# Performance work log

Measured on AMD Instinct MI355X. Metric: run time of the kernel, lower is better.

Reference implementation:

```python
import jax, jax.numpy as jnp
import numpy as np

DIM = 1024
HEADS = 8
DIM_HEAD = 64
DIM_INNER = HEADS * DIM_HEAD  # 512


def setup_inputs() -> dict:
    key = jax.random.key(0)
    k1, k2, k3, k4 = jax.random.split(key, 4)
    x = jax.random.normal(k1, (1, 4096, DIM), dtype=jnp.float32)
    gamma = jnp.ones((DIM,), dtype=jnp.float32)
    w_qkv = jax.random.normal(k2, (DIM, 3 * DIM_INNER), dtype=jnp.float32) * (DIM ** -0.5)
    w_out = jax.random.normal(k3, (DIM_INNER, DIM), dtype=jnp.float32) * (DIM_INNER ** -0.5)
    return {"x": x, "gamma": gamma, "w_qkv": w_qkv, "w_out": w_out}


def _rmsnorm(x, gamma):
    # F.normalize(x, dim=-1) * sqrt(dim) * gamma
    norm = jnp.sqrt(jnp.sum(x * x, axis=-1, keepdims=True))
    x = x / jnp.maximum(norm, 1e-12)
    return x * (DIM ** 0.5) * gamma


def reference(x, gamma, w_qkv, w_out):
    b, n, _ = x.shape
    h, d = HEADS, DIM_HEAD
    normed = _rmsnorm(x, gamma)
    qkv = normed @ w_qkv  # [b, n, 3*h*d]
    qkv = qkv.reshape(b, n, 3, h, d)
    q = jnp.transpose(qkv[:, :, 0], (0, 2, 1, 3))  # b h n d
    k = jnp.transpose(qkv[:, :, 1], (0, 2, 1, 3))
    v = jnp.transpose(qkv[:, :, 2], (0, 2, 1, 3))
    # default_attention (faithful: scales q by d**0.5 as in source)
    q = q * (d ** 0.5)
    sim = jnp.einsum('bhid,bhjd->bhij', q, k)
    mask_value = -jnp.finfo(sim.dtype).max
    causal_mask = jnp.triu(jnp.ones((n, n), dtype=bool), 1)
    sim = jnp.where(causal_mask, mask_value, sim)
    attn = jax.nn.softmax(sim, axis=-1)
    out = jnp.einsum('bhij,bhjd->bhid', attn, v)  # b h n d
    out = jnp.transpose(out, (0, 2, 1, 3)).reshape(b, n, h * d)
    return out @ w_out  # [b, n, dim]
```

## Files before the change

kernel.cpp:

```cpp
#include <hip/hip_runtime.h>
#include <math.h>

#define SEQ 4096
#define DIM 1024
#define HEADS 8
#define DINNER 512
#define QKVW 1536
#define PAD 80
#define CHUNK 16

typedef unsigned short u16;
typedef __attribute__((ext_vector_type(8))) short s8v;
typedef __attribute__((ext_vector_type(4))) float f4v;
#define MFMA(a, b, c) __builtin_amdgcn_mfma_f32_16x16x32_bf16(a, b, c, 0, 0, 0)

__device__ __forceinline__ u16 f2bf(float f) {
    unsigned u = __float_as_uint(f);
    u += 0x7fff + ((u >> 16) & 1);
    return (u16)(u >> 16);
}
__device__ __forceinline__ float bf2f(u16 b) { return __uint_as_float(((unsigned)b) << 16); }

__device__ __forceinline__ void gload16(const u16* g, u16* l) {
    __builtin_amdgcn_global_load_lds(
        (const __attribute__((address_space(1))) unsigned int*)g,
        (__attribute__((address_space(3))) unsigned int*)l, 16, 0, 0);
}

__device__ __forceinline__ int base16(int qt) {
    int a = qt >> 4, b = qt & 15;
    return 8 * a * (a + 1) + b * (a + 1);
}
__device__ __forceinline__ float* po_sel(int T, float* pd, float* pw) {
    return (T < 1024) ? pd + (size_t)T * 4096 : pw + (size_t)(T - 1024) * 4096;
}

__global__ __launch_bounds__(256) void rmsnorm_split(const float* __restrict__ x,
                                                     const float* __restrict__ gamma,
                                                     u16* __restrict__ hi,
                                                     u16* __restrict__ lo) {
    __shared__ float red[4];
    const int row = blockIdx.x, t = threadIdx.x;
    const float4 xv = ((const float4*)(x + (size_t)row * DIM))[t];
    float ss = xv.x * xv.x + xv.y * xv.y + xv.z * xv.z + xv.w * xv.w;
#pragma unroll
    for (int off = 32; off >= 1; off >>= 1) ss += __shfl_xor(ss, off, 64);
    if ((t & 63) == 0) red[t >> 6] = ss;
    __syncthreads();
    float scale = 32.0f / fmaxf(sqrtf(red[0] + red[1] + red[2] + red[3]), 1e-12f);
    const float4 gv = ((const float4*)gamma)[t];
    float y[4] = {xv.x * scale * gv.x, xv.y * scale * gv.y,
                  xv.z * scale * gv.z, xv.w * scale * gv.w};
    unsigned hw0, hw1, lw0, lw1;
    {
        u16 h0 = f2bf(y[0]), h1 = f2bf(y[1]), h2 = f2bf(y[2]), h3 = f2bf(y[3]);
        hw0 = (unsigned)h0 | ((unsigned)h1 << 16);
        hw1 = (unsigned)h2 | ((unsigned)h3 << 16);
        lw0 = (unsigned)f2bf(y[0] - bf2f(h0)) | ((unsigned)f2bf(y[1] - bf2f(h1)) << 16);
        lw1 = (unsigned)f2bf(y[2] - bf2f(h2)) | ((unsigned)f2bf(y[3] - bf2f(h3)) << 16);
    }
    *(uint2*)&hi[(size_t)row * DIM + t * 4] = make_uint2(hw0, hw1);
    *(uint2*)&lo[(size_t)row * DIM + t * 4] = make_uint2(lw0, lw1);
}

__global__ __launch_bounds__(256) void transpose_split(const float* __restrict__ in,
                                                       u16* __restrict__ hi,
                                                       u16* __restrict__ lo,
                                                       int R, int C, int want_lo) {
    __shared__ float tile[64][65];
    const int c0 = blockIdx.x * 64, r0 = blockIdx.y * 64;
    const int t = threadIdx.x, col = t & 63, rb = t >> 6;
#pragma unroll
    for (int j = 0; j < 16; ++j)
        tile[rb + j * 4][col] = in[(size_t)(r0 + rb + j * 4) * C + c0 + col];
    __syncthreads();
#pragma unroll
    for (int j = 0; j < 16; ++j) {
        int cc = rb + j * 4;
        float v = tile[col][cc];
        size_t oi = (size_t)(c0 + cc) * R + r0 + col;
        u16 h = f2bf(v);
        hi[oi] = h;
        if (want_lo) lo[oi] = f2bf(v - bf2f(h));
    }
}

__global__ __launch_bounds__(256) void gemm_qkv_128(
    const u16* __restrict__ Ah, const u16* __restrict__ Al,
    const u16* __restrict__ Bh, const u16* __restrict__ Bl,
    u16* __restrict__ qh, u16* __restrict__ ql,
    u16* __restrict__ kh, u16* __restrict__ kl, u16* __restrict__ vtp) {
    __shared__ __align__(16) u16 AsH[128 * 64], AsL[128 * 64];
    __shared__ __align__(16) u16 BsH[64 * 64], BsL[64 * 64];
    const int t = threadIdx.x;
    const int bn = blockIdx.x * 64, bm = blockIdx.y * 128;
    const int w = t >> 6, lane = t & 63, m = lane & 15, q = lane >> 4;
    const int wr = w >> 1, wc = w & 1;
    f4v acc[4][2];
#pragma unroll
    for (int i = 0; i < 4; ++i)
#pragma unroll
        for (int j = 0; j < 2; ++j) acc[i][j] = (f4v){0.f, 0.f, 0.f, 0.f};

    for (int k0 = 0; k0 < DIM; k0 += 64) {
        __syncthreads();
#pragma unroll
        for (int i = 0; i < 4; ++i) {
            int idx0 = i * 256 + w * 64;
            int row = (idx0 + lane) >> 3;
            int col = ((lane & 7) * 8) ^ ((row & 7) * 8);
            gload16(&Ah[(size_t)(bm + row) * DIM + k0 + col], &AsH[idx0 * 8]);
            gload16(&Al[(size_t)(bm + row) * DIM + k0 + col], &AsL[idx0 * 8]);
            if (i < 2) {
                gload16(&Bh[(size_t)(bn + row) * DIM + k0 + col], &BsH[idx0 * 8]);
                gload16(&Bl[(size_t)(bn + row) * DIM + k0 + col], &BsL[idx0 * 8]);
            }
        }
        __syncthreads();
#pragma unroll
        for (int kk = 0; kk < 64; kk += 32) {
            s8v a_h[4], a_l[4], b_h[2], b_l[2];
#pragma unroll
            for (int f = 0; f < 4; ++f) {
                int ar = wr * 64 + f * 16 + m;
                int ab = ar * 128 + (((kk + q * 8) * 2) ^ ((ar & 7) << 4));
                a_h[f] = *(const s8v*)((const char*)AsH + ab);
                a_l[f] = *(const s8v*)((const char*)AsL + ab);
            }
#pragma unroll
            for (int f = 0; f < 2; ++f) {
                int br = wc * 32 + f * 16 + m;
                int bb = br * 128 + (((kk + q * 8) * 2) ^ ((br & 7) << 4));
                b_h[f] = *(const s8v*)((const char*)BsH + bb);
                b_l[f] = *(const s8v*)((const char*)BsL + bb);
            }
#pragma unroll
            for (int fm = 0; fm < 4; ++fm)
#pragma unroll
                for (int fn = 0; fn < 2; ++fn) {
                    acc[fm][fn] = MFMA(a_h[fm], b_h[fn], acc[fm][fn]);
                    acc[fm][fn] = MFMA(a_l[fm], b_h[fn], acc[fm][fn]);
                    acc[fm][fn] = MFMA(a_h[fm], b_l[fn], acc[fm][fn]);
                }
        }
    }
    const int region = bn >> 9;
#pragma unroll
    for (int fm = 0; fm < 4; ++fm)
#pragma unroll
        for (int fn = 0; fn < 2; ++fn)
#pragma unroll
            for (int r = 0; r < 4; ++r) {
                int gr = bm + wr * 64 + fm * 16 + q * 4 + r;
                int gc = bn + wc * 32 + fn * 16 + m;
                float v = acc[fm][fn][r];
                if (region == 0) {
                    v *= 8.0f;
                    u16 h = f2bf(v);
                    qh[(size_t)gr * DINNER + gc] = h;
                    ql[(size_t)gr * DINNER + gc] = f2bf(v - bf2f(h));
                } else if (region == 1) {
                    u16 h = f2bf(v);
                    kh[(size_t)gr * DINNER + (gc - 512)] = h;
                    kl[(size_t)gr * DINNER + (gc - 512)] = f2bf(v - bf2f(h));
                } else {
                    vtp[(size_t)(gc - 1024) * SEQ + gr] = f2bf(v);
                }
            }
}

__global__ __launch_bounds__(256) void attn_chunk(
    const u16* __restrict__ qhp, const u16* __restrict__ qlp,
    const u16* __restrict__ kh, const u16* __restrict__ kl,
    const u16* __restrict__ vt,
    float* __restrict__ po_dout, float* __restrict__ po_wqt,
    float* __restrict__ ml) {
    __shared__ __align__(16) u16 KH[2][64 * 64], KL[2][64 * 64], VT[2][64 * 64];
    const int t = threadIdx.x;
    const int bx = blockIdx.x;
    const int qt = 63 - (bx >> 2), c = bx & 3, h = blockIdx.y;
    if (c * CHUNK > qt) return;
    const int kt0 = c * CHUNK;
    const int kt1 = (qt < kt0 + CHUNK - 1) ? qt : (kt0 + CHUNK - 1);
    const int w = t >> 6, lane = t & 63, m = lane & 15, g = lane >> 4;

    const size_t qrow = (size_t)(qt * 64 + w * 16 + m) * DINNER + h * 64;
    const s8v qf_h0 = *(const s8v*)&qhp[qrow + g * 8];
    const s8v qf_h1 = *(const s8v*)&qhp[qrow + 32 + g * 8];
    const s8v qf_l0 = *(const s8v*)&qlp[qrow + g * 8];
    const s8v qf_l1 = *(const s8v*)&qlp[qrow + 32 + g * 8];

    const int sg0a = w * 64, sg0b = 256 + w * 64;
    const int srowa = (sg0a + lane) >> 3, srowb = (sg0b + lane) >> 3;
    const int sca = ((lane & 7) ^ (srowa & 7)) * 8;
    const int scb = ((lane & 7) ^ (srowb & 7)) * 8;

    f4v o[4] = {{0.f, 0.f, 0.f, 0.f}, {0.f, 0.f, 0.f, 0.f},
                {0.f, 0.f, 0.f, 0.f}, {0.f, 0.f, 0.f, 0.f}};
    float mi_s = -1e30f, li_s = 0.f;

    {
        const u16* kr = &kh[(size_t)(kt0 * 64) * DINNER + h * 64];
        const u16* lr = &kl[(size_t)(kt0 * 64) * DINNER + h * 64];
        const u16* vr = &vt[(size_t)(h * 64) * SEQ + kt0 * 64];
        gload16(kr + (size_t)srowa * DINNER + sca, &KH[0][sg0a * 8]);
        gload16(kr + (size_t)srowb * DINNER + scb, &KH[0][sg0b * 8]);
        gload16(lr + (size_t)srowa * DINNER + sca, &KL[0][sg0a * 8]);
        gload16(lr + (size_t)srowb * DINNER + scb, &KL[0][sg0b * 8]);
        gload16(vr + (size_t)srowa * SEQ + sca, &VT[0][sg0a * 8]);
        gload16(vr + (size_t)srowb * SEQ + scb, &VT[0][sg0b * 8]);
    }
    __syncthreads();

    int cur = 0;
    for (int kt = kt0; kt <= kt1; ++kt) {
        if (kt < kt1) {
            int nb = cur ^ 1;
            const u16* kr = &kh[(size_t)((kt + 1) * 64) * DINNER + h * 64];
            const u16* lr = &kl[(size_t)((kt + 1) * 64) * DINNER + h * 64];
            const u16* vr = &vt[(size_t)(h * 64) * SEQ + (kt + 1) * 64];
            gload16(kr + (size_t)srowa * DINNER + sca, &KH[nb][sg0a * 8]);
            gload16(kr + (size_t)srowb * DINNER + scb, &KH[nb][sg0b * 8]);
            gload16(lr + (size_t)srowa * DINNER + sca, &KL[nb][sg0a * 8]);
            gload16(lr + (size_t)srowb * DINNER + scb, &KL[nb][sg0b * 8]);
            gload16(vr + (size_t)srowa * SEQ + sca, &VT[nb][sg0a * 8]);
            gload16(vr + (size_t)srowb * SEQ + scb, &VT[nb][sg0b * 8]);
        }

        const char* KHc = (const char*)KH[cur];
        const char* KLc = (const char*)KL[cur];
        f4v s[4] = {{0.f, 0.f, 0.f, 0.f}, {0.f, 0.f, 0.f, 0.f},
                    {0.f, 0.f, 0.f, 0.f}, {0.f, 0.f, 0.f, 0.f}};
#pragma unroll
        for (int ct = 0; ct < 4; ++ct) {
            int rr = ct * 16 + m, rb = rr * 128, sw = (rr & 7) << 4;
            s8v bh0 = *(const s8v*)(KHc + rb + ((g * 16) ^ sw));
            s8v bl0 = *(const s8v*)(KLc + rb + ((g * 16) ^ sw));
            s[ct] = MFMA(bh0, qf_h0, s[ct]);
            s[ct] = MFMA(bh0, qf_l0, s[ct]);
            s[ct] = MFMA(bl0, qf_h0, s[ct]);
            s8v bh1 = *(const s8v*)(KHc + rb + ((64 + g * 16) ^ sw));
            s8v bl1 = *(const s8v*)(KLc + rb + ((64 + g * 16) ^ sw));
            s[ct] = MFMA(bh1, qf_h1, s[ct]);
            s[ct] = MFMA(bh1, qf_l1, s[ct]);
            s[ct] = MFMA(bl1, qf_h1, s[ct]);
        }
        if (kt == qt) {
#pragma unroll
            for (int ct = 0; ct < 4; ++ct)
#pragma unroll
                for (int r = 0; r < 4; ++r)
                    if (ct * 16 + g * 4 + r > w * 16 + m) s[ct][r] = -1e30f;
        }

        float rm = -1e30f;
#pragma unroll
        for (int ct = 0; ct < 4; ++ct)
#pragma unroll
            for (int r = 0; r < 4; ++r) rm = fmaxf(rm, s[ct][r]);
        rm = fmaxf(rm, __shfl_xor(rm, 16, 64));
        rm = fmaxf(rm, __shfl_xor(rm, 32, 64));
        float mn = fmaxf(mi_s, rm);
        float al = __expf(mi_s - mn);
        mi_s = mn;
        float rs = 0.f;
#pragma unroll
        for (int ct = 0; ct < 4; ++ct)
#pragma unroll
            for (int r = 0; r < 4; ++r) {
                s[ct][r] = __expf(s[ct][r] - mn);
                rs += s[ct][r];
            }
        rs += __shfl_xor(rs, 16, 64);
        rs += __shfl_xor(rs, 32, 64);
        li_s = li_s * al + rs;
        float alo[4];
#pragma unroll
        for (int r = 0; r < 4; ++r) alo[r] = __shfl(al, g * 4 + r, 64);

        __syncthreads();

        const int pr = w * 16 + m, pb = pr * 128, psw = (pr & 7) << 4;
#pragma unroll
        for (int ct = 0; ct < 4; ++ct) {
            unsigned w0 = (unsigned)f2bf(s[ct][0]) | ((unsigned)f2bf(s[ct][1]) << 16);
            unsigned w1 = (unsigned)f2bf(s[ct][2]) | ((unsigned)f2bf(s[ct][3]) << 16);
            *(uint2*)((char*)KH[cur] + pb + ((ct * 32 + g * 8) ^ psw)) = make_uint2(w0, w1);
        }
#pragma unroll
        for (int ct = 0; ct < 4; ++ct)
#pragma unroll
            for (int r = 0; r < 4; ++r) o[ct][r] *= alo[r];
#pragma unroll
        for (int kk = 0; kk < 2; ++kk) {
            s8v ap = *(const s8v*)((const char*)KH[cur] + pb + ((kk * 64 + g * 16) ^ psw));
#pragma unroll
            for (int ct = 0; ct < 4; ++ct) {
                int vr2 = ct * 16 + m;
                s8v bv = *(const s8v*)((const char*)VT[cur] + vr2 * 128 +
                                       ((kk * 64 + g * 16) ^ ((vr2 & 7) << 4)));
                o[ct] = MFMA(ap, bv, o[ct]);
            }
        }
        __syncthreads();
        cur ^= 1;
    }

    const int T = h * 160 + base16(qt) + c;
    float* po = po_sel(T, po_dout, po_wqt);
#pragma unroll
    for (int ct = 0; ct < 4; ++ct)
#pragma unroll
        for (int r = 0; r < 4; ++r)
            po[(size_t)(w * 16 + g * 4 + r) * 64 + ct * 16 + m] = o[ct][r];
    if (g == 0) {
        ml[(size_t)T * 128 + w * 16 + m] = mi_s;
        ml[(size_t)T * 128 + 64 + w * 16 + m] = li_s;
    }
}

__global__ __launch_bounds__(256) void attn_merge(
    float* __restrict__ po_dout, float* __restrict__ po_wqt,
    const float* __restrict__ ml, u16* __restrict__ atto) {
    const int qt = blockIdx.x, h = blockIdx.y;
    const int nc = (qt >> 4) + 1;
    const int t = threadIdx.x, col = t & 63, rg = t >> 6;
    const int T0 = h * 160 + base16(qt);
    for (int j = 0; j < 16; ++j) {
        int row = rg * 16 + j;
        float mv[4], lv[4], M = -1e30f;
#pragma unroll 4
        for (int cc = 0; cc < 4; ++cc)
            if (cc < nc) {
                mv[cc] = ml[(size_t)(T0 + cc) * 128 + row];
                lv[cc] = ml[(size_t)(T0 + cc) * 128 + 64 + row];
                M = fmaxf(M, mv[cc]);
            }
        float acc = 0.f, den = 0.f;
#pragma unroll 4
        for (int cc = 0; cc < 4; ++cc)
            if (cc < nc) {
                const float* po = po_sel(T0 + cc, po_dout, po_wqt);
                float wg = __expf(mv[cc] - M);
                den += lv[cc] * wg;
                acc += wg * po[(size_t)row * 64 + col];
            }
        atto[(size_t)(qt * 64 + row) * DINNER + h * 64 + col] = f2bf(acc / den);
    }
}

__global__ __launch_bounds__(256) void attn_mfma(
    const u16* __restrict__ qh, const u16* __restrict__ ql,
    const u16* __restrict__ kh, const u16* __restrict__ kl,
    const u16* __restrict__ vt, u16* __restrict__ atto) {
    __shared__ u16 Qh[64 * PAD], Ql[64 * PAD], KP[64 * PAD], Kl[64 * PAD], Vt[64 * PAD];
    const int t = threadIdx.x;
    const int qt = blockIdx.x, h = blockIdx.y;
    const int w = t >> 6, lane = t & 63, m = lane & 15, q = lane >> 4;

#pragma unroll
    for (int i = 0; i < 2; ++i) {
        int c = t + i * 256, row = c >> 3, ch = (c & 7) * 8;
        *(uint4*)&Qh[row * PAD + ch] =
            *(const uint4*)&qh[(size_t)(qt * 64 + row) * DINNER + h * 64 + ch];
        *(uint4*)&Ql[row * PAD + ch] =
            *(const uint4*)&ql[(size_t)(qt * 64 + row) * DINNER + h * 64 + ch];
    }

    f4v o[4] = {{0.f, 0.f, 0.f, 0.f}, {0.f, 0.f, 0.f, 0.f},
                {0.f, 0.f, 0.f, 0.f}, {0.f, 0.f, 0.f, 0.f}};
    float mi[4] = {-1e30f, -1e30f, -1e30f, -1e30f};
    float li[4] = {0.f, 0.f, 0.f, 0.f};

    for (int kt = 0; kt <= qt; ++kt) {
        __syncthreads();
#pragma unroll
        for (int i = 0; i < 2; ++i) {
            int c = t + i * 256, row = c >> 3, ch = (c & 7) * 8;
            *(uint4*)&KP[row * PAD + ch] =
                *(const uint4*)&kh[(size_t)(kt * 64 + row) * DINNER + h * 64 + ch];
            *(uint4*)&Kl[row * PAD + ch] =
                *(const uint4*)&kl[(size_t)(kt * 64 + row) * DINNER + h * 64 + ch];
            *(uint4*)&Vt[row * PAD + ch] =
                *(const uint4*)&vt[(size_t)(h * 64 + row) * SEQ + kt * 64 + ch];
        }
        __syncthreads();

        f4v s[4] = {{0.f, 0.f, 0.f, 0.f}, {0.f, 0.f, 0.f, 0.f},
                    {0.f, 0.f, 0.f, 0.f}, {0.f, 0.f, 0.f, 0.f}};
#pragma unroll
        for (int kk = 0; kk < 64; kk += 32) {
            s8v ah = *(const s8v*)&Qh[(w * 16 + m) * PAD + kk + q * 8];
            s8v al = *(const s8v*)&Ql[(w * 16 + m) * PAD + kk + q * 8];
#pragma unroll
            for (int ct = 0; ct < 4; ++ct) {
                s8v bh = *(const s8v*)&KP[(ct * 16 + m) * PAD + kk + q * 8];
                s8v bl = *(const s8v*)&Kl[(ct * 16 + m) * PAD + kk + q * 8];
                s[ct] = MFMA(ah, bh, s[ct]);
                s[ct] = MFMA(al, bh, s[ct]);
                s[ct] = MFMA(ah, bl, s[ct]);
            }
        }
        if (kt == qt) {
#pragma unroll
            for (int ct = 0; ct < 4; ++ct)
#pragma unroll
                for (int r = 0; r < 4; ++r)
                    if (ct * 16 + m > w * 16 + q * 4 + r) s[ct][r] = -1e30f;
        }

        float alpha[4];
#pragma unroll
        for (int r = 0; r < 4; ++r) {
            float rm = fmaxf(fmaxf(s[0][r], s[1][r]), fmaxf(s[2][r], s[3][r]));
#pragma unroll
            for (int off = 8; off >= 1; off >>= 1) rm = fmaxf(rm, __shfl_xor(rm, off, 64));
            float mn = fmaxf(mi[r], rm);
            alpha[r] = __expf(mi[r] - mn);
            mi[r] = mn;
            float rs = 0.f;
#pragma unroll
            for (int ct = 0; ct < 4; ++ct) {
                s[ct][r] = __expf(s[ct][r] - mn);
                rs += s[ct][r];
            }
#pragma unroll
            for (int off = 8; off >= 1; off >>= 1) rs += __shfl_xor(rs, off, 64);
            li[r] = li[r] * alpha[r] + rs;
        }

        __syncthreads();
#pragma unroll
        for (int ct = 0; ct < 4; ++ct)
#pragma unroll
            for (int r = 0; r < 4; ++r) {
                KP[(w * 16 + q * 4 + r) * PAD + ct * 16 + m] = f2bf(s[ct][r]);
                o[ct][r] *= alpha[r];
            }
#pragma unroll
        for (int kk = 0; kk < 64; kk += 32) {
            s8v ap = *(const s8v*)&KP[(w * 16 + m) * PAD + kk + q * 8];
#pragma unroll
            for (int ct = 0; ct < 4; ++ct) {
                s8v bv = *(const s8v*)&Vt[(ct * 16 + m) * PAD + kk + q * 8];
                o[ct] = MFMA(ap, bv, o[ct]);
            }
        }
    }

#pragma unroll
    for (int r = 0; r < 4; ++r) {
        float inv = 1.0f / li[r];
#pragma unroll
        for (int ct = 0; ct < 4; ++ct)
            atto[(size_t)(qt * 64 + w * 16 + q * 4 + r) * DINNER + h * 64 + ct * 16 + m] =
                f2bf(o[ct][r] * inv);
    }
}

__global__ __launch_bounds__(256) void gemm_out_128(const u16* __restrict__ A,
                                                    const u16* __restrict__ Bt,
                                                    float* __restrict__ C) {
    __shared__ __align__(16) u16 As[128 * 64], Bs[64 * 64];
    const int t = threadIdx.x;
    const int bn = blockIdx.x * 64, bm = blockIdx.y * 128;
    const int w = t >> 6, lane = t & 63, m = lane & 15, q = lane >> 4;
    const int wr = w >> 1, wc = w & 1;
    f4v acc[4][2];
#pragma unroll
    for (int i = 0; i < 4; ++i)
#pragma unroll
        for (int j = 0; j < 2; ++j) acc[i][j] = (f4v){0.f, 0.f, 0.f, 0.f};

    for (int k0 = 0; k0 < DINNER; k0 += 64) {
        __syncthreads();
#pragma unroll
        for (int i = 0; i < 4; ++i) {
            int idx0 = i * 256 + w * 64;
            int row = (idx0 + lane) >> 3;
            int col = ((lane & 7) * 8) ^ ((row & 7) * 8);
            gload16(&A[(size_t)(bm + row) * DINNER + k0 + col], &As[idx0 * 8]);
            if (i < 2)
                gload16(&Bt[(size_t)(bn + row) * DINNER + k0 + col], &Bs[idx0 * 8]);
        }
        __syncthreads();
#pragma unroll
        for (int kk = 0; kk < 64; kk += 32) {
            s8v a_f[4], b_f[2];
#pragma unroll
            for (int f = 0; f < 4; ++f) {
                int ar = wr * 64 + f * 16 + m;
                a_f[f] = *(const s8v*)((const char*)As + ar * 128 +
                                       (((kk + q * 8) * 2) ^ ((ar & 7) << 4)));
            }
#pragma unroll
            for (int f = 0; f < 2; ++f) {
                int br = wc * 32 + f * 16 + m;
                b_f[f] = *(const s8v*)((const char*)Bs + br * 128 +
                                       (((kk + q * 8) * 2) ^ ((br & 7) << 4)));
            }
#pragma unroll
            for (int fm = 0; fm < 4; ++fm)
#pragma unroll
                for (int fn = 0; fn < 2; ++fn)
                    acc[fm][fn] = MFMA(a_f[fm], b_f[fn], acc[fm][fn]);
        }
    }
#pragma unroll
    for (int fm = 0; fm < 4; ++fm)
#pragma unroll
        for (int fn = 0; fn < 2; ++fn)
#pragma unroll
            for (int r = 0; r < 4; ++r)
                C[(size_t)(bm + wr * 64 + fm * 16 + q * 4 + r) * DIM +
                  bn + wc * 32 + fn * 16 + m] = acc[fm][fn][r];
}

extern "C" void kernel_launch(void* const* d_in, const int* in_sizes, int n_in,
                              void* d_out, int out_size, void* d_ws, size_t ws_size,
                              hipStream_t stream) {
    const float* x     = (const float*)d_in[0];
    const float* gamma = (const float*)d_in[1];
    const float* w_qkv = (const float*)d_in[2];
    const float* w_out = (const float*)d_in[3];
    float* out = (float*)d_out;

    u16* nh = (u16*)d_out;
    u16* nl = nh + (size_t)SEQ * DIM;

    u16* p = (u16*)d_ws;
    u16* wqt_h = p; p += (size_t)QKVW * DIM;
    u16* wqt_l = p; p += (size_t)QKVW * DIM;
    u16* wot   = p; p += (size_t)DIM * DINNER;
    u16* qh = p; p += (size_t)SEQ * DINNER;
    u16* ql = p; p += (size_t)SEQ * DINNER;
    u16* kh = p; p += (size_t)SEQ * DINNER;
    u16* kl = p; p += (size_t)SEQ * DINNER;
    u16* vt = p; p += (size_t)DINNER * SEQ;
    u16* atto = p; p += (size_t)SEQ * DINNER;

    float* po_dout = (float*)d_out;
    float* po_wqt  = (float*)wqt_h;
    float* ml      = (float*)p;
    const size_t need = (size_t)((char*)(ml + (size_t)1280 * 128) - (char*)d_ws);
    const bool split = ws_size >= need;

    transpose_split<<<dim3(QKVW / 64, DIM / 64), 256, 0, stream>>>(w_qkv, wqt_h, wqt_l,
                                                                   DIM, QKVW, 1);
    transpose_split<<<dim3(DIM / 64, DINNER / 64), 256, 0, stream>>>(w_out, wot, nullptr,
                                                                     DINNER, DIM, 0);
    rmsnorm_split<<<SEQ, 256, 0, stream>>>(x, gamma, nh, nl);
    gemm_qkv_128<<<dim3(QKVW / 64, SEQ / 128), 256, 0, stream>>>(nh, nl, wqt_h, wqt_l,
                                                                 qh, ql, kh, kl, vt);
    if (split) {
        attn_chunk<<<dim3(256, HEADS), 256, 0, stream>>>(qh, ql, kh, kl, vt,
                                                         po_dout, po_wqt, ml);
        attn_merge<<<dim3(SEQ / 64, HEADS), 256, 0, stream>>>(po_dout, po_wqt, ml, atto);
    } else {
        attn_mfma<<<dim3(SEQ / 64, HEADS), 256, 0, stream>>>(qh, ql, kh, kl, vt, atto);
    }
    gemm_out_128<<<dim3(DIM / 64, SEQ / 128), 256, 0, stream>>>(atto, wot, out);
}
```

Before: 289.2 us.

## Process two query tiles per attention block to reuse staged K/V tiles

Each attn_chunk block now handles two adjacent 64-row query tiles, sharing each K/V tile loaded into LDS between both, and the grid is halved. This halves global-to-LDS traffic and barrier count per unit of work, and gives more MFMA work between synchronisations. In exchange, register pressure rises (two sets of Q fragments and accumulators), fewer blocks are launched, and the KL buffer is reused as the P staging area for the second tile.

```diff
diff --git a/kernel.cpp b/kernel.cpp
--- a/kernel.cpp
+++ b/kernel.cpp
@@ -178,26 +178,34 @@
     __shared__ __align__(16) u16 KH[2][64 * 64], KL[2][64 * 64], VT[2][64 * 64];
     const int t = threadIdx.x;
     const int bx = blockIdx.x;
-    const int qt = 63 - (bx >> 2), c = bx & 3, h = blockIdx.y;
-    if (c * CHUNK > qt) return;
+    const int j = 31 - (bx >> 2), c = bx & 3, h = blockIdx.y;
+    if (8 * c > j) return;
+    const int qtA = 2 * j, qtB = 2 * j + 1;
     const int kt0 = c * CHUNK;
-    const int kt1 = (qt < kt0 + CHUNK - 1) ? qt : (kt0 + CHUNK - 1);
+    const int kt1 = (qtB < kt0 + CHUNK - 1) ? qtB : (kt0 + CHUNK - 1);
     const int w = t >> 6, lane = t & 63, m = lane & 15, g = lane >> 4;
 
-    const size_t qrow = (size_t)(qt * 64 + w * 16 + m) * DINNER + h * 64;
-    const s8v qf_h0 = *(const s8v*)&qhp[qrow + g * 8];
-    const s8v qf_h1 = *(const s8v*)&qhp[qrow + 32 + g * 8];
-    const s8v qf_l0 = *(const s8v*)&qlp[qrow + g * 8];
-    const s8v qf_l1 = *(const s8v*)&qlp[qrow + 32 + g * 8];
+    const size_t qrowA = (size_t)(qtA * 64 + w * 16 + m) * DINNER + h * 64;
+    const size_t qrowB = (size_t)(qtB * 64 + w * 16 + m) * DINNER + h * 64;
+    const s8v qA_h0 = *(const s8v*)&qhp[qrowA + g * 8];
+    const s8v qA_h1 = *(const s8v*)&qhp[qrowA + 32 + g * 8];
+    const s8v qA_l0 = *(const s8v*)&qlp[qrowA + g * 8];
+    const s8v qA_l1 = *(const s8v*)&qlp[qrowA + 32 + g * 8];
+    const s8v qB_h0 = *(const s8v*)&qhp[qrowB + g * 8];
+    const s8v qB_h1 = *(const s8v*)&qhp[qrowB + 32 + g * 8];
+    const s8v qB_l0 = *(const s8v*)&qlp[qrowB + g * 8];
+    const s8v qB_l1 = *(const s8v*)&qlp[qrowB + 32 + g * 8];
 
     const int sg0a = w * 64, sg0b = 256 + w * 64;
     const int srowa = (sg0a + lane) >> 3, srowb = (sg0b + lane) >> 3;
     const int sca = ((lane & 7) ^ (srowa & 7)) * 8;
     const int scb = ((lane & 7) ^ (srowb & 7)) * 8;
 
-    f4v o[4] = {{0.f, 0.f, 0.f, 0.f}, {0.f, 0.f, 0.f, 0.f},
-                {0.f, 0.f, 0.f, 0.f}, {0.f, 0.f, 0.f, 0.f}};
-    float mi_s = -1e30f, li_s = 0.f;
+    f4v oA[4] = {{0.f, 0.f, 0.f, 0.f}, {0.f, 0.f, 0.f, 0.f},
+                 {0.f, 0.f, 0.f, 0.f}, {0.f, 0.f, 0.f, 0.f}};
+    f4v oB[4] = {{0.f, 0.f, 0.f, 0.f}, {0.f, 0.f, 0.f, 0.f},
+                 {0.f, 0.f, 0.f, 0.f}, {0.f, 0.f, 0.f, 0.f}};
+    float miA = -1e30f, liA = 0.f, miB = -1e30f, liB = 0.f;
 
     {
         const u16* kr = &kh[(size_t)(kt0 * 64) * DINNER + h * 64];
@@ -229,93 +237,181 @@
 
         const char* KHc = (const char*)KH[cur];
         const char* KLc = (const char*)KL[cur];
-        f4v s[4] = {{0.f, 0.f, 0.f, 0.f}, {0.f, 0.f, 0.f, 0.f},
-                    {0.f, 0.f, 0.f, 0.f}, {0.f, 0.f, 0.f, 0.f}};
-#pragma unroll
-        for (int ct = 0; ct < 4; ++ct) {
-            int rr = ct * 16 + m, rb = rr * 128, sw = (rr & 7) << 4;
-            s8v bh0 = *(const s8v*)(KHc + rb + ((g * 16) ^ sw));
-            s8v bl0 = *(const s8v*)(KLc + rb + ((g * 16) ^ sw));
-            s[ct] = MFMA(bh0, qf_h0, s[ct]);
-            s[ct] = MFMA(bh0, qf_l0, s[ct]);
-            s[ct] = MFMA(bl0, qf_h0, s[ct]);
-            s8v bh1 = *(const s8v*)(KHc + rb + ((64 + g * 16) ^ sw));
-            s8v bl1 = *(const s8v*)(KLc + rb + ((64 + g * 16) ^ sw));
-            s[ct] = MFMA(bh1, qf_h1, s[ct]);
-            s[ct] = MFMA(bh1, qf_l1, s[ct]);
-            s[ct] = MFMA(bl1, qf_h1, s[ct]);
-        }
-        if (kt == qt) {
-#pragma unroll
-            for (int ct = 0; ct < 4; ++ct)
-#pragma unroll
-                for (int r = 0; r < 4; ++r)
-                    if (ct * 16 + g * 4 + r > w * 16 + m) s[ct][r] = -1e30f;
-        }
-
-        float rm = -1e30f;
-#pragma unroll
-        for (int ct = 0; ct < 4; ++ct)
-#pragma unroll
-            for (int r = 0; r < 4; ++r) rm = fmaxf(rm, s[ct][r]);
-        rm = fmaxf(rm, __shfl_xor(rm, 16, 64));
-        rm = fmaxf(rm, __shfl_xor(rm, 32, 64));
-        float mn = fmaxf(mi_s, rm);
-        float al = __expf(mi_s - mn);
-        mi_s = mn;
-        float rs = 0.f;
-#pragma unroll
-        for (int ct = 0; ct < 4; ++ct)
-#pragma unroll
-            for (int r = 0; r < 4; ++r) {
-                s[ct][r] = __expf(s[ct][r] - mn);
-                rs += s[ct][r];
-            }
-        rs += __shfl_xor(rs, 16, 64);
-        rs += __shfl_xor(rs, 32, 64);
-        li_s = li_s * al + rs;
-        float alo[4];
-#pragma unroll
-        for (int r = 0; r < 4; ++r) alo[r] = __shfl(al, g * 4 + r, 64);
+        const bool doA = (kt <= qtA);
+        uint2 paA[4], paB[4];
+        float aloA[4], aloB[4];
+
+        if (doA) {
+            f4v s[4] = {{0.f, 0.f, 0.f, 0.f}, {0.f, 0.f, 0.f, 0.f},
+                        {0.f, 0.f, 0.f, 0.f}, {0.f, 0.f, 0.f, 0.f}};
+#pragma unroll
+            for (int ct = 0; ct < 4; ++ct) {
+                int rr = ct * 16 + m, rb = rr * 128, sw = (rr & 7) << 4;
+                s8v bh0 = *(const s8v*)(KHc + rb + ((g * 16) ^ sw));
+                s8v bl0 = *(const s8v*)(KLc + rb + ((g * 16) ^ sw));
+                s[ct] = MFMA(bh0, qA_h0, s[ct]);
+                s[ct] = MFMA(bh0, qA_l0, s[ct]);
+                s[ct] = MFMA(bl0, qA_h0, s[ct]);
+                s8v bh1 = *(const s8v*)(KHc + rb + ((64 + g * 16) ^ sw));
+                s8v bl1 = *(const s8v*)(KLc + rb + ((64 + g * 16) ^ sw));
+                s[ct] = MFMA(bh1, qA_h1, s[ct]);
+                s[ct] = MFMA(bh1, qA_l1, s[ct]);
+                s[ct] = MFMA(bl1, qA_h1, s[ct]);
+            }
+            if (kt == qtA) {
+#pragma unroll
+                for (int ct = 0; ct < 4; ++ct)
+#pragma unroll
+                    for (int r = 0; r < 4; ++r)
+                        if (ct * 16 + g * 4 + r > w * 16 + m) s[ct][r] = -1e30f;
+            }
+            float rm = -1e30f;
+#pragma unroll
+            for (int ct = 0; ct < 4; ++ct)
+#pragma unroll
+                for (int r = 0; r < 4; ++r) rm = fmaxf(rm, s[ct][r]);
+            rm = fmaxf(rm, __shfl_xor(rm, 16, 64));
+            rm = fmaxf(rm, __shfl_xor(rm, 32, 64));
+            float mn = fmaxf(miA, rm);
+            float al = __expf(miA - mn);
+            miA = mn;
+            float rs = 0.f;
+#pragma unroll
+            for (int ct = 0; ct < 4; ++ct)
+#pragma unroll
+                for (int r = 0; r < 4; ++r) {
+                    s[ct][r] = __expf(s[ct][r] - mn);
+                    rs += s[ct][r];
+                }
+            rs += __shfl_xor(rs, 16, 64);
+            rs += __shfl_xor(rs, 32, 64);
+            liA = liA * al + rs;
+#pragma unroll
+            for (int r = 0; r < 4; ++r) aloA[r] = __shfl(al, g * 4 + r, 64);
+#pragma unroll
+            for (int ct = 0; ct < 4; ++ct)
+                paA[ct] = make_uint2(
+                    (unsigned)f2bf(s[ct][0]) | ((unsigned)f2bf(s[ct][1]) << 16),
+                    (unsigned)f2bf(s[ct][2]) | ((unsigned)f2bf(s[ct][3]) << 16));
+        }
+
+        {
+            f4v s[4] = {{0.f, 0.f, 0.f, 0.f}, {0.f, 0.f, 0.f, 0.f},
+                        {0.f, 0.f, 0.f, 0.f}, {0.f, 0.f, 0.f, 0.f}};
+#pragma unroll
+            for (int ct = 0; ct < 4; ++ct) {
+                int rr = ct * 16 + m, rb = rr * 128, sw = (rr & 7) << 4;
+                s8v bh0 = *(const s8v*)(KHc + rb + ((g * 16) ^ sw));
+                s8v bl0 = *(const s8v*)(KLc + rb + ((g * 16) ^ sw));
+                s[ct] = MFMA(bh0, qB_h0, s[ct]);
+                s[ct] = MFMA(bh0, qB_l0, s[ct]);
+                s[ct] = MFMA(bl0, qB_h0, s[ct]);
+                s8v bh1 = *(const s8v*)(KHc + rb + ((64 + g * 16) ^ sw));
+                s8v bl1 = *(const s8v*)(KLc + rb + ((64 + g * 16) ^ sw));
+                s[ct] = MFMA(bh1, qB_h1, s[ct]);
+                s[ct] = MFMA(bh1, qB_l1, s[ct]);
+                s[ct] = MFMA(bl1, qB_h1, s[ct]);
+            }
+            if (kt == qtB) {
+#pragma unroll
+                for (int ct = 0; ct < 4; ++ct)
+#pragma unroll
+                    for (int r = 0; r < 4; ++r)
+                        if (ct * 16 + g * 4 + r > w * 16 + m) s[ct][r] = -1e30f;
+            }
+            float rm = -1e30f;
+#pragma unroll
+            for (int ct = 0; ct < 4; ++ct)
+#pragma unroll
+                for (int r = 0; r < 4; ++r) rm = fmaxf(rm, s[ct][r]);
+            rm = fmaxf(rm, __shfl_xor(rm, 16, 64));
+            rm = fmaxf(rm, __shfl_xor(rm, 32, 64));
+            float mn = fmaxf(miB, rm);
+            float al = __expf(miB - mn);
+            miB = mn;
+            float rs = 0.f;
+#pragma unroll
+            for (int ct = 0; ct < 4; ++ct)
+#pragma unroll
+                for (int r = 0; r < 4; ++r) {
+                    s[ct][r] = __expf(s[ct][r] - mn);
+                    rs += s[ct][r];
+                }
+            rs += __shfl_xor(rs, 16, 64);
+            rs += __shfl_xor(rs, 32, 64);
+            liB = liB * al + rs;
+#pragma unroll
+            for (int r = 0; r < 4; ++r) aloB[r] = __shfl(al, g * 4 + r, 64);
+#pragma unroll
+            for (int ct = 0; ct < 4; ++ct)
+                paB[ct] = make_uint2(
+                    (unsigned)f2bf(s[ct][0]) | ((unsigned)f2bf(s[ct][1]) << 16),
+                    (unsigned)f2bf(s[ct][2]) | ((unsigned)f2bf(s[ct][3]) << 16));
+        }
 
         __syncthreads();
 
         const int pr = w * 16 + m, pb = pr * 128, psw = (pr & 7) << 4;
-#pragma unroll
-        for (int ct = 0; ct < 4; ++ct) {
-            unsigned w0 = (unsigned)f2bf(s[ct][0]) | ((unsigned)f2bf(s[ct][1]) << 16);
-            unsigned w1 = (unsigned)f2bf(s[ct][2]) | ((unsigned)f2bf(s[ct][3]) << 16);
-            *(uint2*)((char*)KH[cur] + pb + ((ct * 32 + g * 8) ^ psw)) = make_uint2(w0, w1);
-        }
-#pragma unroll
-        for (int ct = 0; ct < 4; ++ct)
-#pragma unroll
-            for (int r = 0; r < 4; ++r) o[ct][r] *= alo[r];
-#pragma unroll
-        for (int kk = 0; kk < 2; ++kk) {
-            s8v ap = *(const s8v*)((const char*)KH[cur] + pb + ((kk * 64 + g * 16) ^ psw));
-#pragma unroll
-            for (int ct = 0; ct < 4; ++ct) {
-                int vr2 = ct * 16 + m;
-                s8v bv = *(const s8v*)((const char*)VT[cur] + vr2 * 128 +
-                                       ((kk * 64 + g * 16) ^ ((vr2 & 7) << 4)));
-                o[ct] = MFMA(ap, bv, o[ct]);
+        if (doA) {
+#pragma unroll
+            for (int ct = 0; ct < 4; ++ct)
+                *(uint2*)((char*)KH[cur] + pb + ((ct * 32 + g * 8) ^ psw)) = paA[ct];
+#pragma unroll
+            for (int ct = 0; ct < 4; ++ct)
+#pragma unroll
+                for (int r = 0; r < 4; ++r) oA[ct][r] *= aloA[r];
+#pragma unroll
+            for (int kk = 0; kk < 2; ++kk) {
+                s8v ap = *(const s8v*)((const char*)KH[cur] + pb + ((kk * 64 + g * 16) ^ psw));
+#pragma unroll
+                for (int ct = 0; ct < 4; ++ct) {
+                    int vr2 = ct * 16 + m;
+                    s8v bv = *(const s8v*)((const char*)VT[cur] + vr2 * 128 +
+                                           ((kk * 64 + g * 16) ^ ((vr2 & 7) << 4)));
+                    oA[ct] = MFMA(ap, bv, oA[ct]);
+                }
+            }
+        }
+        {
+#pragma unroll
+            for (int ct = 0; ct < 4; ++ct)
+                *(uint2*)((char*)KL[cur] + pb + ((ct * 32 + g * 8) ^ psw)) = paB[ct];
+#pragma unroll
+            for (int ct = 0; ct < 4; ++ct)
+#pragma unroll
+                for (int r = 0; r < 4; ++r) oB[ct][r] *= aloB[r];
+#pragma unroll
+            for (int kk = 0; kk < 2; ++kk) {
+                s8v ap = *(const s8v*)((const char*)KL[cur] + pb + ((kk * 64 + g * 16) ^ psw));
+#pragma unroll
+                for (int ct = 0; ct < 4; ++ct) {
+                    int vr2 = ct * 16 + m;
+                    s8v bv = *(const s8v*)((const char*)VT[cur] + vr2 * 128 +
+                                           ((kk * 64 + g * 16) ^ ((vr2 & 7) << 4)));
+                    oB[ct] = MFMA(ap, bv, oB[ct]);
+                }
             }
         }
         __syncthreads();
         cur ^= 1;
     }
 
-    const int T = h * 160 + base16(qt) + c;
-    float* po = po_sel(T, po_dout, po_wqt);
+    const int TA = h * 160 + base16(qtA) + c;
+    const int TB = h * 160 + base16(qtB) + c;
+    float* poA = po_sel(TA, po_dout, po_wqt);
+    float* poB = po_sel(TB, po_dout, po_wqt);
 #pragma unroll
     for (int ct = 0; ct < 4; ++ct)
 #pragma unroll
-        for (int r = 0; r < 4; ++r)
-            po[(size_t)(w * 16 + g * 4 + r) * 64 + ct * 16 + m] = o[ct][r];
+        for (int r = 0; r < 4; ++r) {
+            poA[(size_t)(w * 16 + g * 4 + r) * 64 + ct * 16 + m] = oA[ct][r];
+            poB[(size_t)(w * 16 + g * 4 + r) * 64 + ct * 16 + m] = oB[ct][r];
+        }
     if (g == 0) {
-        ml[(size_t)T * 128 + w * 16 + m] = mi_s;
-        ml[(size_t)T * 128 + 64 + w * 16 + m] = li_s;
+        ml[(size_t)TA * 128 + w * 16 + m] = miA;
+        ml[(size_t)TA * 128 + 64 + w * 16 + m] = liA;
+        ml[(size_t)TB * 128 + w * 16 + m] = miB;
+        ml[(size_t)TB * 128 + 64 + w * 16 + m] = liB;
     }
 }
 
@@ -553,7 +649,7 @@
     gemm_qkv_128<<<dim3(QKVW / 64, SEQ / 128), 256, 0, stream>>>(nh, nl, wqt_h, wqt_l,
                                                                  qh, ql, kh, kl, vt);
     if (split) {
-        attn_chunk<<<dim3(256, HEADS), 256, 0, stream>>>(qh, ql, kh, kl, vt,
+        attn_chunk<<<dim3(128, HEADS), 256, 0, stream>>>(qh, ql, kh, kl, vt,
                                                          po_dout, po_wqt, ml);
         attn_merge<<<dim3(SEQ / 64, HEADS), 256, 0, stream>>>(po_dout, po_wqt, ml, atto);
     } else {
```

After: 281.3 us. 1.03x faster.

## Load K/V fragments straight from global memory and drop shared-memory staging

Applied to the files above, without the earlier changes.

The attention chunk kernel no longer stages K-high, K-low and V^T tiles into double-buffered shared memory with async global-to-LDS loads. Each wave now reads its MFMA operands directly from global memory. Only a small per-wave padded buffer for the probability tile stays in shared memory, which lets both block-wide barriers go. The trade-off is that every wave fetches the full K/V tile, roughly four times the global/L2 traffic, and nothing prefetches the next tile, so load latency is exposed. The 68-element padded row stride also leaves 16-byte LDS reads only 8-byte aligned.

```diff
diff --git a/kernel.cpp b/kernel.cpp
--- a/kernel.cpp
+++ b/kernel.cpp
@@ -175,7 +175,7 @@
     const u16* __restrict__ vt,
     float* __restrict__ po_dout, float* __restrict__ po_wqt,
     float* __restrict__ ml) {
-    __shared__ __align__(16) u16 KH[2][64 * 64], KL[2][64 * 64], VT[2][64 * 64];
+    __shared__ u16 P[64 * 68];
     const int t = threadIdx.x;
     const int bx = blockIdx.x;
     const int qt = 63 - (bx >> 2), c = bx & 3, h = blockIdx.y;
@@ -190,57 +190,29 @@
     const s8v qf_l0 = *(const s8v*)&qlp[qrow + g * 8];
     const s8v qf_l1 = *(const s8v*)&qlp[qrow + 32 + g * 8];
 
-    const int sg0a = w * 64, sg0b = 256 + w * 64;
-    const int srowa = (sg0a + lane) >> 3, srowb = (sg0b + lane) >> 3;
-    const int sca = ((lane & 7) ^ (srowa & 7)) * 8;
-    const int scb = ((lane & 7) ^ (srowb & 7)) * 8;
-
     f4v o[4] = {{0.f, 0.f, 0.f, 0.f}, {0.f, 0.f, 0.f, 0.f},
                 {0.f, 0.f, 0.f, 0.f}, {0.f, 0.f, 0.f, 0.f}};
     float mi_s = -1e30f, li_s = 0.f;
 
-    {
-        const u16* kr = &kh[(size_t)(kt0 * 64) * DINNER + h * 64];
-        const u16* lr = &kl[(size_t)(kt0 * 64) * DINNER + h * 64];
-        const u16* vr = &vt[(size_t)(h * 64) * SEQ + kt0 * 64];
-        gload16(kr + (size_t)srowa * DINNER + sca, &KH[0][sg0a * 8]);
-        gload16(kr + (size_t)srowb * DINNER + scb, &KH[0][sg0b * 8]);
-        gload16(lr + (size_t)srowa * DINNER + sca, &KL[0][sg0a * 8]);
-        gload16(lr + (size_t)srowb * DINNER + scb, &KL[0][sg0b * 8]);
-        gload16(vr + (size_t)srowa * SEQ + sca, &VT[0][sg0a * 8]);
-        gload16(vr + (size_t)srowb * SEQ + scb, &VT[0][sg0b * 8]);
-    }
-    __syncthreads();
-
-    int cur = 0;
+    u16* Pw = &P[(w * 16 + m) * 68];
+
     for (int kt = kt0; kt <= kt1; ++kt) {
-        if (kt < kt1) {
-            int nb = cur ^ 1;
-            const u16* kr = &kh[(size_t)((kt + 1) * 64) * DINNER + h * 64];
-            const u16* lr = &kl[(size_t)((kt + 1) * 64) * DINNER + h * 64];
-            const u16* vr = &vt[(size_t)(h * 64) * SEQ + (kt + 1) * 64];
-            gload16(kr + (size_t)srowa * DINNER + sca, &KH[nb][sg0a * 8]);
-            gload16(kr + (size_t)srowb * DINNER + scb, &KH[nb][sg0b * 8]);
-            gload16(lr + (size_t)srowa * DINNER + sca, &KL[nb][sg0a * 8]);
-            gload16(lr + (size_t)srowb * DINNER + scb, &KL[nb][sg0b * 8]);
-            gload16(vr + (size_t)srowa * SEQ + sca, &VT[nb][sg0a * 8]);
-            gload16(vr + (size_t)srowb * SEQ + scb, &VT[nb][sg0b * 8]);
-        }
-
-        const char* KHc = (const char*)KH[cur];
-        const char* KLc = (const char*)KL[cur];
+        const u16* kb = kh + (size_t)(kt * 64 + m) * DINNER + h * 64 + g * 8;
+        const u16* lb = kl + (size_t)(kt * 64 + m) * DINNER + h * 64 + g * 8;
+
         f4v s[4] = {{0.f, 0.f, 0.f, 0.f}, {0.f, 0.f, 0.f, 0.f},
                     {0.f, 0.f, 0.f, 0.f}, {0.f, 0.f, 0.f, 0.f}};
 #pragma unroll
         for (int ct = 0; ct < 4; ++ct) {
-            int rr = ct * 16 + m, rb = rr * 128, sw = (rr & 7) << 4;
-            s8v bh0 = *(const s8v*)(KHc + rb + ((g * 16) ^ sw));
-            s8v bl0 = *(const s8v*)(KLc + rb + ((g * 16) ^ sw));
+            const u16* kr = kb + (size_t)(ct * 16) * DINNER;
+            const u16* lr = lb + (size_t)(ct * 16) * DINNER;
+            s8v bh0 = *(const s8v*)kr;
+            s8v bl0 = *(const s8v*)lr;
+            s8v bh1 = *(const s8v*)(kr + 32);
+            s8v bl1 = *(const s8v*)(lr + 32);
             s[ct] = MFMA(bh0, qf_h0, s[ct]);
             s[ct] = MFMA(bh0, qf_l0, s[ct]);
             s[ct] = MFMA(bl0, qf_h0, s[ct]);
-            s8v bh1 = *(const s8v*)(KHc + rb + ((64 + g * 16) ^ sw));
-            s8v bl1 = *(const s8v*)(KLc + rb + ((64 + g * 16) ^ sw));
             s[ct] = MFMA(bh1, qf_h1, s[ct]);
             s[ct] = MFMA(bh1, qf_l1, s[ct]);
             s[ct] = MFMA(bl1, qf_h1, s[ct]);
@@ -278,32 +250,27 @@
 #pragma unroll
         for (int r = 0; r < 4; ++r) alo[r] = __shfl(al, g * 4 + r, 64);
 
-        __syncthreads();
-
-        const int pr = w * 16 + m, pb = pr * 128, psw = (pr & 7) << 4;
 #pragma unroll
         for (int ct = 0; ct < 4; ++ct) {
             unsigned w0 = (unsigned)f2bf(s[ct][0]) | ((unsigned)f2bf(s[ct][1]) << 16);
             unsigned w1 = (unsigned)f2bf(s[ct][2]) | ((unsigned)f2bf(s[ct][3]) << 16);
-            *(uint2*)((char*)KH[cur] + pb + ((ct * 32 + g * 8) ^ psw)) = make_uint2(w0, w1);
+            *(uint2*)&Pw[ct * 16 + g * 4] = make_uint2(w0, w1);
         }
 #pragma unroll
         for (int ct = 0; ct < 4; ++ct)
 #pragma unroll
             for (int r = 0; r < 4; ++r) o[ct][r] *= alo[r];
+
+        const u16* vb = vt + (size_t)(h * 64 + m) * SEQ + kt * 64 + g * 8;
 #pragma unroll
         for (int kk = 0; kk < 2; ++kk) {
-            s8v ap = *(const s8v*)((const char*)KH[cur] + pb + ((kk * 64 + g * 16) ^ psw));
+            s8v ap = *(const s8v*)&Pw[kk * 32 + g * 8];
 #pragma unroll
             for (int ct = 0; ct < 4; ++ct) {
-                int vr2 = ct * 16 + m;
-                s8v bv = *(const s8v*)((const char*)VT[cur] + vr2 * 128 +
-                                       ((kk * 64 + g * 16) ^ ((vr2 & 7) << 4)));
+                s8v bv = *(const s8v*)(vb + (size_t)(ct * 16) * SEQ + kk * 32);
                 o[ct] = MFMA(ap, bv, o[ct]);
             }
         }
-        __syncthreads();
-        cur ^= 1;
     }
 
     const int T = h * 160 + base16(qt) + c;
```

Result: slower. 519.0 us (+79.4%).
